# Kernel optimization log

Hardware: AMD Instinct MI355X
Metric: run time of the kernel (lower is better)

The kernel has to match this reference:

```python
import jax, jax.numpy as jnp
import numpy as np

TEMPERATURE = 0.5
EPS = 1e-12  # matches F.normalize eps


def setup_inputs() -> dict:
    key = jax.random.key(0)
    k1, k2 = jax.random.split(key)
    B, D = 4096, 128
    z_i = jax.random.normal(k1, (B, D), dtype=jnp.float32)
    z_j = jax.random.normal(k2, (B, D), dtype=jnp.float32)
    return {"z_i": z_i, "z_j": z_j}


def _l2_normalize(x):
    # F.normalize(x, dim=1): x / max(||x||, eps)
    norm = jnp.sqrt(jnp.sum(x * x, axis=1, keepdims=True))
    return x / jnp.maximum(norm, EPS)


def reference(z_i, z_j):
    B = z_i.shape[0]
    zi = _l2_normalize(z_i)
    zj = _l2_normalize(z_j)
    z = jnp.concatenate([zi, zj], axis=0)  # [2B, D], rows unit-norm
    # cosine similarity of unit vectors == dot product
    sim = jnp.matmul(z, z.T) / TEMPERATURE  # [2B, 2B]
    # Removing the diagonal and shifting columns (as in the torch code) is
    # equivalent, for cross-entropy, to masking the diagonal with -inf: the
    # diagonal contributes exp(-inf)=0 to logsumexp and labels never hit it.
    n = 2 * B
    diag = jnp.eye(n, dtype=bool)
    logits = jnp.where(diag, -jnp.inf, sim)
    # positive for row i (<B) is column i+B; for row i+B it is column i
    ar = jnp.arange(B)
    labels = jnp.concatenate([ar + B, ar])  # indices in the FULL matrix
    lse = jax.nn.logsumexp(logits, axis=1)  # [2B]
    pos = sim[jnp.arange(n), labels]  # positive logits (never on diag)
    loss = jnp.sum(lse - pos) / n
    return loss
```

## Files before the change

kernel.cpp:

```cpp
#include <hip/hip_runtime.h>
#include <hip/hip_bf16.h>
#include <math.h>

#define B_ROWS 4096
#define N_ROWS 8192
#define D 128
#define INV_T 2.0f
#define CHUNKS 8
#define JT_PER_CHUNK 8

typedef __attribute__((ext_vector_type(8))) short bf16x8;
typedef __attribute__((ext_vector_type(4))) float f32x4;

__global__ __launch_bounds__(256) void normalize_kernel(
    const float* __restrict__ z_i, const float* __restrict__ z_j,
    ushort* __restrict__ Z) {
  const int wave = threadIdx.x >> 6;
  const int lane = threadIdx.x & 63;
  const int row = blockIdx.x * 4 + wave;
  const float* src = (row < B_ROWS) ? (z_i + (size_t)row * D)
                                    : (z_j + (size_t)(row - B_ROWS) * D);
  float2 v = *(const float2*)(src + lane * 2);
  float ss = v.x * v.x + v.y * v.y;
#pragma unroll
  for (int off = 32; off > 0; off >>= 1) ss += __shfl_xor(ss, off);
  float scale = 1.0f / fmaxf(sqrtf(ss), 1e-12f);
  __hip_bfloat16 h0 = __float2bfloat16(v.x * scale);
  __hip_bfloat16 h1 = __float2bfloat16(v.y * scale);
  ushort2 o;
  o.x = *(ushort*)&h0;
  o.y = *(ushort*)&h1;
  *(ushort2*)(Z + (size_t)row * D + lane * 2) = o;
}

__global__ __launch_bounds__(256) void sim_kernel(
    const ushort* __restrict__ Z, float* __restrict__ partials,
    float* __restrict__ pos_buf) {
  const int t = threadIdx.x;
  const int lane = t & 63;
  const int w = t >> 6;
  const int wy = w >> 1, wx = w & 1;
  const int l15 = lane & 15;
  const int l4 = lane >> 4;
  const int row0 = blockIdx.x * 128;
  const int chunk = blockIdx.y;

  bf16x8 a[4][4];
  const int arow = row0 + wy * 64 + l15;
#pragma unroll
  for (int rs = 0; rs < 4; ++rs)
#pragma unroll
    for (int ks = 0; ks < 4; ++ks)
      a[rs][ks] = *(const bf16x8*)(Z + (size_t)(arow + rs * 16) * D + ks * 32 + l4 * 8);

  float rowsum[4][4];
#pragma unroll
  for (int rs = 0; rs < 4; ++rs)
#pragma unroll
    for (int r = 0; r < 4; ++r) rowsum[rs][r] = 0.f;

  for (int jt = 0; jt < JT_PER_CHUNK; ++jt) {
    const int colb = chunk * 1024 + jt * 128 + wx * 64;
#pragma unroll
    for (int cs = 0; cs < 4; ++cs) {
      bf16x8 b[4];
      const int bcol = colb + cs * 16 + l15;
#pragma unroll
      for (int ks = 0; ks < 4; ++ks)
        b[ks] = *(const bf16x8*)(Z + (size_t)bcol * D + ks * 32 + l4 * 8);

      f32x4 c[4];
#pragma unroll
      for (int rs = 0; rs < 4; ++rs) c[rs] = (f32x4){0.f, 0.f, 0.f, 0.f};
#pragma unroll
      for (int ks = 0; ks < 4; ++ks)
#pragma unroll
        for (int rs = 0; rs < 4; ++rs)
          c[rs] = __builtin_amdgcn_mfma_f32_16x16x32_bf16(a[rs][ks], b[ks], c[rs], 0, 0, 0);

      const int gj = colb + cs * 16 + l15;
#pragma unroll
      for (int rs = 0; rs < 4; ++rs) {
        const int gibase = row0 + wy * 64 + rs * 16 + l4 * 4;
#pragma unroll
        for (int reg = 0; reg < 4; ++reg) {
          const int gi = gibase + reg;
          float s = c[rs][reg] * INV_T;
          float e = __expf(s);
          rowsum[rs][reg] += (gi != gj) ? e : 0.f;
          if ((gi ^ gj) == B_ROWS) pos_buf[gi] = s;
        }
      }
    }
  }

#pragma unroll
  for (int rs = 0; rs < 4; ++rs)
#pragma unroll
    for (int r = 0; r < 4; ++r) {
      float v = rowsum[rs][r];
      v += __shfl_xor(v, 1);
      v += __shfl_xor(v, 2);
      v += __shfl_xor(v, 4);
      v += __shfl_xor(v, 8);
      rowsum[rs][r] = v;
    }

  __shared__ float rs_lds[128];
  if (wx == 0 && l15 == 0) {
#pragma unroll
    for (int rs = 0; rs < 4; ++rs)
#pragma unroll
      for (int r = 0; r < 4; ++r)
        rs_lds[wy * 64 + rs * 16 + l4 * 4 + r] = rowsum[rs][r];
  }
  __syncthreads();
  if (wx == 1 && l15 == 0) {
#pragma unroll
    for (int rs = 0; rs < 4; ++rs)
#pragma unroll
      for (int r = 0; r < 4; ++r)
        rs_lds[wy * 64 + rs * 16 + l4 * 4 + r] += rowsum[rs][r];
  }
  __syncthreads();
  if (t < 128)
    partials[(size_t)(row0 + t) * CHUNKS + chunk] = rs_lds[t];
}

__global__ __launch_bounds__(128) void reduce1_kernel(
    const float* __restrict__ partials, const float* __restrict__ pos_buf,
    float* __restrict__ loss_part) {
  const int row = blockIdx.x * 128 + threadIdx.x;
  float tot = 0.f;
#pragma unroll
  for (int c = 0; c < CHUNKS; ++c) tot += partials[(size_t)row * CHUNKS + c];
  float term = logf(tot) - pos_buf[row];
#pragma unroll
  for (int off = 32; off > 0; off >>= 1) term += __shfl_xor(term, off);
  __shared__ float wsum[2];
  if ((threadIdx.x & 63) == 0) wsum[threadIdx.x >> 6] = term;
  __syncthreads();
  if (threadIdx.x == 0) loss_part[blockIdx.x] = wsum[0] + wsum[1];
}

__global__ __launch_bounds__(64) void reduce2_kernel(
    const float* __restrict__ loss_part, float* __restrict__ out) {
  float v = loss_part[threadIdx.x];
#pragma unroll
  for (int off = 32; off > 0; off >>= 1) v += __shfl_xor(v, off);
  if (threadIdx.x == 0) out[0] = v / (float)N_ROWS;
}

extern "C" void kernel_launch(void* const* d_in, const int* in_sizes, int n_in,
                              void* d_out, int out_size, void* d_ws, size_t ws_size,
                              hipStream_t stream) {
  const float* z_i = (const float*)d_in[0];
  const float* z_j = (const float*)d_in[1];
  float* out = (float*)d_out;

  ushort* Z = (ushort*)d_ws;
  float* partials = (float*)((char*)d_ws + (size_t)N_ROWS * D * sizeof(ushort));
  float* pos_buf = partials + (size_t)N_ROWS * CHUNKS;
  float* loss_part = pos_buf + N_ROWS;

  hipLaunchKernelGGL(normalize_kernel, dim3(N_ROWS / 4), dim3(256), 0, stream,
                     z_i, z_j, Z);
  hipLaunchKernelGGL(sim_kernel, dim3(N_ROWS / 128, CHUNKS), dim3(256), 0,
                     stream, Z, partials, pos_buf);
  hipLaunchKernelGGL(reduce1_kernel, dim3(N_ROWS / 128), dim3(128), 0, stream,
                     partials, pos_buf, loss_part);
  hipLaunchKernelGGL(reduce2_kernel, dim3(1), dim3(64), 0, stream, loss_part,
                     out);
}
```

Before: 103.9 us.

## Exploit symmetry of similarity matrix and compute positives in normalize kernel

The similarity matrix is symmetric, so only upper-triangular 128x128 tiles are computed. Each off-diagonal tile contributes both row sums and column sums to a per-tile partials array. Positive logits are now computed in fp32 during normalization as a direct dot product, which removes the scattered pos_buf writes from the hot loop, and exp is replaced with exp2 using a folded constant. The trade-offs are a 64x64 grid in which about half the blocks exit immediately, a larger partials buffer that the final reduction must read with 64 loads per row, and extra shuffles for the column sums.

Measured after the change: 130.6 us. +25.6%, slower.

```diff
diff --git a/kernel.cpp b/kernel.cpp
--- a/kernel.cpp
+++ b/kernel.cpp
@@ -5,92 +5,121 @@
 #define B_ROWS 4096
 #define N_ROWS 8192
 #define D 128
-#define INV_T 2.0f
-#define CHUNKS 8
-#define JT_PER_CHUNK 8
+#define NT 64
 
 typedef __attribute__((ext_vector_type(8))) short bf16x8;
 typedef __attribute__((ext_vector_type(4))) float f32x4;
 
-__global__ __launch_bounds__(256) void normalize_kernel(
+#if __has_builtin(__builtin_amdgcn_exp2f)
+#define EXP2(x) __builtin_amdgcn_exp2f(x)
+#else
+#define EXP2(x) exp2f(x)
+#endif
+#define K2 2.8853900818f
+
+__global__ __launch_bounds__(256) void normalize_pos_kernel(
     const float* __restrict__ z_i, const float* __restrict__ z_j,
-    ushort* __restrict__ Z) {
+    ushort* __restrict__ Z, float* __restrict__ pos_buf) {
   const int wave = threadIdx.x >> 6;
   const int lane = threadIdx.x & 63;
-  const int row = blockIdx.x * 4 + wave;
-  const float* src = (row < B_ROWS) ? (z_i + (size_t)row * D)
-                                    : (z_j + (size_t)(row - B_ROWS) * D);
-  float2 v = *(const float2*)(src + lane * 2);
-  float ss = v.x * v.x + v.y * v.y;
-#pragma unroll
-  for (int off = 32; off > 0; off >>= 1) ss += __shfl_xor(ss, off);
-  float scale = 1.0f / fmaxf(sqrtf(ss), 1e-12f);
-  __hip_bfloat16 h0 = __float2bfloat16(v.x * scale);
-  __hip_bfloat16 h1 = __float2bfloat16(v.y * scale);
-  ushort2 o;
-  o.x = *(ushort*)&h0;
-  o.y = *(ushort*)&h1;
-  *(ushort2*)(Z + (size_t)row * D + lane * 2) = o;
+  const int r = blockIdx.x * 4 + wave;
+  float2 vi = *(const float2*)(z_i + (size_t)r * D + lane * 2);
+  float2 vj = *(const float2*)(z_j + (size_t)r * D + lane * 2);
+  float ssi = vi.x * vi.x + vi.y * vi.y;
+  float ssj = vj.x * vj.x + vj.y * vj.y;
+  float cr = vi.x * vj.x + vi.y * vj.y;
+#pragma unroll
+  for (int off = 32; off > 0; off >>= 1) {
+    ssi += __shfl_xor(ssi, off);
+    ssj += __shfl_xor(ssj, off);
+    cr += __shfl_xor(cr, off);
+  }
+  float si = 1.0f / fmaxf(sqrtf(ssi), 1e-12f);
+  float sj = 1.0f / fmaxf(sqrtf(ssj), 1e-12f);
+  __hip_bfloat16 a0 = __float2bfloat16(vi.x * si);
+  __hip_bfloat16 a1 = __float2bfloat16(vi.y * si);
+  __hip_bfloat16 b0 = __float2bfloat16(vj.x * sj);
+  __hip_bfloat16 b1 = __float2bfloat16(vj.y * sj);
+  ushort2 oi, oj;
+  oi.x = *(ushort*)&a0; oi.y = *(ushort*)&a1;
+  oj.x = *(ushort*)&b0; oj.y = *(ushort*)&b1;
+  *(ushort2*)(Z + (size_t)r * D + lane * 2) = oi;
+  *(ushort2*)(Z + (size_t)(r + B_ROWS) * D + lane * 2) = oj;
+  if (lane == 0) {
+    float pos = 2.0f * cr * si * sj;
+    pos_buf[r] = pos;
+    pos_buf[r + B_ROWS] = pos;
+  }
 }
 
 __global__ __launch_bounds__(256) void sim_kernel(
-    const ushort* __restrict__ Z, float* __restrict__ partials,
-    float* __restrict__ pos_buf) {
+    const ushort* __restrict__ Z, float* __restrict__ partials) {
+  const int ti = blockIdx.x, tj = blockIdx.y;
+  if (ti > tj) return;
+  const bool isdiag = (ti == tj);
   const int t = threadIdx.x;
   const int lane = t & 63;
   const int w = t >> 6;
   const int wy = w >> 1, wx = w & 1;
   const int l15 = lane & 15;
   const int l4 = lane >> 4;
-  const int row0 = blockIdx.x * 128;
-  const int chunk = blockIdx.y;
 
   bf16x8 a[4][4];
-  const int arow = row0 + wy * 64 + l15;
+  const int arow = ti * 128 + wy * 64 + l15;
 #pragma unroll
   for (int rs = 0; rs < 4; ++rs)
 #pragma unroll
     for (int ks = 0; ks < 4; ++ks)
       a[rs][ks] = *(const bf16x8*)(Z + (size_t)(arow + rs * 16) * D + ks * 32 + l4 * 8);
 
-  float rowsum[4][4];
+  float rowacc[4][4];
 #pragma unroll
   for (int rs = 0; rs < 4; ++rs)
 #pragma unroll
-    for (int r = 0; r < 4; ++r) rowsum[rs][r] = 0.f;
-
-  for (int jt = 0; jt < JT_PER_CHUNK; ++jt) {
-    const int colb = chunk * 1024 + jt * 128 + wx * 64;
-#pragma unroll
-    for (int cs = 0; cs < 4; ++cs) {
-      bf16x8 b[4];
-      const int bcol = colb + cs * 16 + l15;
-#pragma unroll
-      for (int ks = 0; ks < 4; ++ks)
-        b[ks] = *(const bf16x8*)(Z + (size_t)bcol * D + ks * 32 + l4 * 8);
-
-      f32x4 c[4];
-#pragma unroll
-      for (int rs = 0; rs < 4; ++rs) c[rs] = (f32x4){0.f, 0.f, 0.f, 0.f};
-#pragma unroll
-      for (int ks = 0; ks < 4; ++ks)
-#pragma unroll
-        for (int rs = 0; rs < 4; ++rs)
-          c[rs] = __builtin_amdgcn_mfma_f32_16x16x32_bf16(a[rs][ks], b[ks], c[rs], 0, 0, 0);
-
-      const int gj = colb + cs * 16 + l15;
+    for (int r = 0; r < 4; ++r) rowacc[rs][r] = 0.f;
+  float colacc[4] = {0.f, 0.f, 0.f, 0.f};
+
+#pragma unroll
+  for (int cs = 0; cs < 4; ++cs) {
+    const int bcol = tj * 128 + wx * 64 + cs * 16 + l15;
+    bf16x8 b[4];
+#pragma unroll
+    for (int ks = 0; ks < 4; ++ks)
+      b[ks] = *(const bf16x8*)(Z + (size_t)bcol * D + ks * 32 + l4 * 8);
+
+    f32x4 c[4];
+#pragma unroll
+    for (int rs = 0; rs < 4; ++rs) c[rs] = (f32x4){0.f, 0.f, 0.f, 0.f};
+#pragma unroll
+    for (int ks = 0; ks < 4; ++ks)
+#pragma unroll
+      for (int rs = 0; rs < 4; ++rs)
+        c[rs] = __builtin_amdgcn_mfma_f32_16x16x32_bf16(a[rs][ks], b[ks], c[rs], 0, 0, 0);
+
+    if (isdiag) {
+      const int gj = tj * 128 + wx * 64 + cs * 16 + l15;
 #pragma unroll
       for (int rs = 0; rs < 4; ++rs) {
-        const int gibase = row0 + wy * 64 + rs * 16 + l4 * 4;
+        const int gibase = ti * 128 + wy * 64 + rs * 16 + l4 * 4;
 #pragma unroll
         for (int reg = 0; reg < 4; ++reg) {
-          const int gi = gibase + reg;
-          float s = c[rs][reg] * INV_T;
-          float e = __expf(s);
-          rowsum[rs][reg] += (gi != gj) ? e : 0.f;
-          if ((gi ^ gj) == B_ROWS) pos_buf[gi] = s;
+          float e = EXP2(c[rs][reg] * K2);
+          rowacc[rs][reg] += (gibase + reg != gj) ? e : 0.f;
         }
       }
+    } else {
+      float coltmp = 0.f;
+#pragma unroll
+      for (int rs = 0; rs < 4; ++rs)
+#pragma unroll
+        for (int reg = 0; reg < 4; ++reg) {
+          float e = EXP2(c[rs][reg] * K2);
+          rowacc[rs][reg] += e;
+          coltmp += e;
+        }
+      coltmp += __shfl_xor(coltmp, 16);
+      coltmp += __shfl_xor(coltmp, 32);
+      colacc[cs] = coltmp;
     }
   }
 
@@ -98,21 +127,26 @@
   for (int rs = 0; rs < 4; ++rs)
 #pragma unroll
     for (int r = 0; r < 4; ++r) {
-      float v = rowsum[rs][r];
+      float v = rowacc[rs][r];
       v += __shfl_xor(v, 1);
       v += __shfl_xor(v, 2);
       v += __shfl_xor(v, 4);
       v += __shfl_xor(v, 8);
-      rowsum[rs][r] = v;
+      rowacc[rs][r] = v;
     }
 
-  __shared__ float rs_lds[128];
+  __shared__ float rowled[128];
+  __shared__ float colled[128];
   if (wx == 0 && l15 == 0) {
 #pragma unroll
     for (int rs = 0; rs < 4; ++rs)
 #pragma unroll
       for (int r = 0; r < 4; ++r)
-        rs_lds[wy * 64 + rs * 16 + l4 * 4 + r] = rowsum[rs][r];
+        rowled[wy * 64 + rs * 16 + l4 * 4 + r] = rowacc[rs][r];
+  }
+  if (!isdiag && wy == 0 && l4 == 0) {
+#pragma unroll
+    for (int cs = 0; cs < 4; ++cs) colled[wx * 64 + cs * 16 + l15] = colacc[cs];
   }
   __syncthreads();
   if (wx == 1 && l15 == 0) {
@@ -120,21 +154,28 @@
     for (int rs = 0; rs < 4; ++rs)
 #pragma unroll
       for (int r = 0; r < 4; ++r)
-        rs_lds[wy * 64 + rs * 16 + l4 * 4 + r] += rowsum[rs][r];
+        rowled[wy * 64 + rs * 16 + l4 * 4 + r] += rowacc[rs][r];
+  }
+  if (!isdiag && wy == 1 && l4 == 0) {
+#pragma unroll
+    for (int cs = 0; cs < 4; ++cs) colled[wx * 64 + cs * 16 + l15] += colacc[cs];
   }
   __syncthreads();
+
   if (t < 128)
-    partials[(size_t)(row0 + t) * CHUNKS + chunk] = rs_lds[t];
-}
-
-__global__ __launch_bounds__(128) void reduce1_kernel(
+    partials[(size_t)tj * N_ROWS + ti * 128 + t] = rowled[t];
+  else if (!isdiag)
+    partials[(size_t)ti * N_ROWS + tj * 128 + (t - 128)] = colled[t - 128];
+}
+
+__global__ __launch_bounds__(128) void fin1_kernel(
     const float* __restrict__ partials, const float* __restrict__ pos_buf,
     float* __restrict__ loss_part) {
   const int row = blockIdx.x * 128 + threadIdx.x;
   float tot = 0.f;
 #pragma unroll
-  for (int c = 0; c < CHUNKS; ++c) tot += partials[(size_t)row * CHUNKS + c];
-  float term = logf(tot) - pos_buf[row];
+  for (int k = 0; k < NT; ++k) tot += partials[(size_t)k * N_ROWS + row];
+  float term = __logf(tot) - pos_buf[row];
 #pragma unroll
   for (int off = 32; off > 0; off >>= 1) term += __shfl_xor(term, off);
   __shared__ float wsum[2];
@@ -143,7 +184,7 @@
   if (threadIdx.x == 0) loss_part[blockIdx.x] = wsum[0] + wsum[1];
 }
 
-__global__ __launch_bounds__(64) void reduce2_kernel(
+__global__ __launch_bounds__(64) void fin2_kernel(
     const float* __restrict__ loss_part, float* __restrict__ out) {
   float v = loss_part[threadIdx.x];
 #pragma unroll
@@ -159,16 +200,15 @@
   float* out = (float*)d_out;
 
   ushort* Z = (ushort*)d_ws;
-  float* partials = (float*)((char*)d_ws + (size_t)N_ROWS * D * sizeof(ushort));
-  float* pos_buf = partials + (size_t)N_ROWS * CHUNKS;
+  float* partials = (float*)((char*)d_ws + (size_t)N_ROWS * D * 2);
+  float* pos_buf = partials + (size_t)NT * N_ROWS;
   float* loss_part = pos_buf + N_ROWS;
 
-  hipLaunchKernelGGL(normalize_kernel, dim3(N_ROWS / 4), dim3(256), 0, stream,
-                     z_i, z_j, Z);
-  hipLaunchKernelGGL(sim_kernel, dim3(N_ROWS / 128, CHUNKS), dim3(256), 0,
-                     stream, Z, partials, pos_buf);
-  hipLaunchKernelGGL(reduce1_kernel, dim3(N_ROWS / 128), dim3(128), 0, stream,
+  hipLaunchKernelGGL(normalize_pos_kernel, dim3(B_ROWS / 4), dim3(256), 0,
+                     stream, z_i, z_j, Z, pos_buf);
+  hipLaunchKernelGGL(sim_kernel, dim3(NT, NT), dim3(256), 0, stream, Z,
+                     partials);
+  hipLaunchKernelGGL(fin1_kernel, dim3(N_ROWS / 128), dim3(128), 0, stream,
                      partials, pos_buf, loss_part);
-  hipLaunchKernelGGL(reduce2_kernel, dim3(1), dim3(64), 0, stream, loss_part,
-                     out);
-}
+  hipLaunchKernelGGL(fin2_kernel, dim3(1), dim3(64), 0, stream, loss_part, out);
+}
```
